# Kernel tuning notes

Measured on AMD Instinct MI355X. Metric: run time of the kernel, lower is better.

The kernel has to match this reference:

```python
import jax, jax.numpy as jnp
import numpy as np

N = 100000      # nodes
E = 1600000     # edges (avg degree 16)
F_IN = 300      # input feature dim
H = 64          # hidden channels
OUT = 20        # output classes
L = 8           # num GCN2Conv layers
ALPHA = 0.1
THETA = 0.5


def setup_inputs() -> dict:
    key = jax.random.key(0)
    ks = jax.random.split(key, 6)
    x = jax.random.normal(ks[0], (N, F_IN), jnp.float32)
    edge_index = jax.random.randint(ks[1], (2, E), 0, N, dtype=jnp.int32)
    edge_weights = jax.random.uniform(ks[2], (E,), jnp.float32)
    W_in = jax.random.normal(ks[3], (F_IN, H), jnp.float32) / np.sqrt(F_IN)
    b_in = jnp.zeros((H,), jnp.float32)
    conv_w = jax.random.normal(ks[4], (L, H, H), jnp.float32) / np.sqrt(H)
    W_out = jax.random.normal(ks[5], (H, OUT), jnp.float32) / np.sqrt(H)
    b_out = jnp.zeros((OUT,), jnp.float32)
    return dict(x=x, edge_index=edge_index, edge_weights=edge_weights,
                W_in=W_in, b_in=b_in, conv_w=conv_w, W_out=W_out, b_out=b_out)


def _gcn_norm(edge_index, edge_weights, n, dtype):
    # add self-loops with weight 1, symmetric normalization (PyG gcn_norm)
    loop = jnp.arange(n, dtype=edge_index.dtype)
    row = jnp.concatenate([edge_index[0], loop])
    col = jnp.concatenate([edge_index[1], loop])
    w = jnp.concatenate([edge_weights, jnp.ones((n,), dtype)])
    deg = jax.ops.segment_sum(w, col, num_segments=n)
    dinv = jnp.where(deg > 0, jax.lax.rsqrt(deg), 0.0).astype(dtype)
    norm = dinv[row] * w * dinv[col]
    return row, col, norm


def reference(x, edge_index, edge_weights, W_in, b_in, conv_w, W_out, b_out):
    n = x.shape[0]
    row, col, norm = _gcn_norm(edge_index, edge_weights, n, x.dtype)
    # eval mode: dropout is identity
    h = jax.nn.relu(x @ W_in + b_in)   # start_with_lin (F_IN != H)
    x0 = h
    num_layers = conv_w.shape[0]
    for l in range(num_layers):
        beta = float(np.log(THETA / (l + 1) + 1.0))
        # A_hat @ h : gather sources, weight by norm, scatter-add to targets
        agg = jax.ops.segment_sum(norm[:, None] * h[row], col, num_segments=n)
        z = (1.0 - ALPHA) * agg + ALPHA * x0  # initial-residual mixing
        h = jax.nn.relu((1.0 - beta) * z + beta * (z @ conv_w[l]))
    return h @ W_out + b_out
```

## Files before the change

### kernel.cpp

```cpp
#include <hip/hip_runtime.h>
#include <hip/hip_fp16.h>
#include <math.h>


#define HID 64
#define FIN 300
#define NOUT 20
#define ALPHA 0.1f
#define DSCALE 262144.0f
#define CNT_SHIFT 25
#define DEG_MASK 0x1FFFFFFu

typedef _Float16 f16;
typedef f16 f16x8 __attribute__((ext_vector_type(8)));
typedef float f32x4 __attribute__((ext_vector_type(4)));

__device__ __forceinline__ float wdec(unsigned v) {
    union { unsigned short u; __half h; } c;
    c.u = (unsigned short)(v >> 17);
    return __half2float(c.h);
}

__device__ __forceinline__ void unpack8(const float4& v, float* f) {
    const __half2* p = reinterpret_cast<const __half2*>(&v);
#pragma unroll
    for (int i = 0; i < 4; ++i) {
        float2 t = __half22float2(p[i]);
        f[2 * i] = t.x;
        f[2 * i + 1] = t.y;
    }
}

__global__ void zero_k(unsigned* __restrict__ p, int nwords) {
    int i = blockIdx.x * blockDim.x + threadIdx.x;
    if (i < nwords) p[i] = 0u;
}

__global__ void accum_k(const int* __restrict__ row, const int* __restrict__ col,
                        const float* __restrict__ w,
                        unsigned* __restrict__ packed8,
                        uint2* __restrict__ rec, int e, int n) {
    int i = blockIdx.x * blockDim.x + threadIdx.x;
    if (i < e) {
        int copy = blockIdx.x & 7;
        int c = col[i], r = row[i];
        float wv = w[i];
        unsigned q = (unsigned)__float2uint_rn(wv * DSCALE);
        unsigned old = atomicAdd(&packed8[(size_t)copy * n + c], (1u << CNT_SHIFT) | q);
        unsigned rank = (old >> CNT_SHIFT) & 0xFFu;
        union { __half h; unsigned short u; } cv;
        cv.h = __float2half(wv);
        rec[i] = make_uint2((unsigned)c | ((unsigned)copy << 17) | (rank << 20),
                            (unsigned)r | ((unsigned)cv.u << 17));
    }
}

__global__ __launch_bounds__(1024) void unpackscan_k(const unsigned* __restrict__ packed8,
                                                     float* __restrict__ dinv,
                                                     unsigned char* __restrict__ off8,
                                                     int* __restrict__ padcnt,
                                                     int* __restrict__ bsum, int n) {
    __shared__ int s[1024];
    int t = threadIdx.x, i = blockIdx.x * 1024 + t;
    int pad = 0;
    if (i < n) {
        unsigned cnt = 0, dsum = 0;
        union { unsigned char b[8]; uint2 u2; } offs;
#pragma unroll
        for (int k = 0; k < 8; ++k) {
            unsigned v = packed8[(size_t)k * n + i];
            offs.b[k] = (unsigned char)cnt;
            cnt += (v >> CNT_SHIFT);
            dsum += (v & DEG_MASK);
        }
        float d = 1.0f + (float)dsum * (1.0f / DSCALE);
        dinv[i] = rsqrtf(d);
        reinterpret_cast<uint2*>(off8)[i] = offs.u2;
        pad = (int)((cnt + 3u) & ~3u);
        padcnt[i] = pad;
    }
    s[t] = pad;
    __syncthreads();
    for (int off = 512; off > 0; off >>= 1) {
        if (t < off) s[t] += s[t + off];
        __syncthreads();
    }
    if (t == 0) bsum[blockIdx.x] = s[0];
}

__global__ void scan2_k(int* __restrict__ bsum, int nb, int* __restrict__ rp, int n) {
    int lane = threadIdx.x;
    int acc = 0;
    for (int base = 0; base < nb; base += 64) {
        int idx = base + lane;
        int orig = (idx < nb) ? bsum[idx] : 0;
        int v = orig;
#pragma unroll
        for (int d = 1; d < 64; d <<= 1) {
            int u = __shfl_up(v, d);
            if (lane >= d) v += u;
        }
        if (idx < nb) bsum[idx] = acc + v - orig;
        acc += __shfl(v, 63);
    }
    if (lane == 0) rp[n] = acc;
}

__global__ __launch_bounds__(1024) void scan3_k(const int* __restrict__ padcnt,
                                                const int* __restrict__ bsum,
                                                int* __restrict__ rp, int n) {
    __shared__ int s[1024];
    int t = threadIdx.x, i = blockIdx.x * 1024 + t;
    int v = (i < n) ? padcnt[i] : 0;
    s[t] = v;
    __syncthreads();
    for (int off = 1; off < 1024; off <<= 1) {
        int u = (t >= off) ? s[t - off] : 0;
        __syncthreads();
        s[t] += u;
        __syncthreads();
    }
    if (i < n) rp[i] = bsum[blockIdx.x] + s[t] - v;
}

__global__ __launch_bounds__(256) void fill_k(const uint2* __restrict__ rec,
                                              const float* __restrict__ dinv,
                                              const int* __restrict__ rp,
                                              const unsigned char* __restrict__ off8,
                                              unsigned* __restrict__ edges,
                                              int e, int n) {
    int xcd = blockIdx.x & 7;
    int lo = (int)(((long long)n * xcd) >> 3);
    int hi = (int)(((long long)n * (xcd + 1)) >> 3);
    int nblk = gridDim.x >> 3;
    int stride = nblk * 256;
    for (int i = (blockIdx.x >> 3) * 256 + threadIdx.x; i < e; i += stride) {
        uint2 rc = rec[i];
        int c = (int)(rc.x & 0x1FFFFu);
        if (c < lo || c >= hi) continue;
        int r = (int)(rc.y & 0x1FFFFu);
        union { unsigned short u; __half h; } ev;
        ev.u = (unsigned short)(rc.y >> 17);
        float nw = (1.0f - ALPHA) * dinv[r] * __half2float(ev.h) * dinv[c];
        union { __half h; unsigned short u; } cv;
        cv.h = __float2half(nw);
        int copy = (int)((rc.x >> 17) & 7u);
        int rank = (int)((rc.x >> 20) & 0xFFu);
        int pos = rp[c] + (int)off8[c * 8 + copy] + rank;
        edges[pos] = ((unsigned)cv.u << 17) | (unsigned)r;
    }
}

__global__ void wt_k(const float* __restrict__ Win, f16* __restrict__ Wt) {
    int i = blockIdx.x * blockDim.x + threadIdx.x;
    if (i < 64 * 320) {
        int c = i / 320, k = i - c * 320;
        Wt[i] = (k < FIN) ? (f16)Win[k * 64 + c] : (f16)0.0f;
    }
}

__global__ __launch_bounds__(256) void gemm_in_k(const float* __restrict__ x,
                                                 const f16* __restrict__ Wt,
                                                 const float* __restrict__ bin,
                                                 __half* __restrict__ x0h, int n) {
    __shared__ f16 As[64 * 72];
    int t = threadIdx.x, lane = t & 63, wv = t >> 6;
    int node0 = blockIdx.x * 64;
    int lr = lane & 15, kg = lane >> 4;
    int fi = t & 15, rowbase = t >> 4;
    f32x4 acc0 = {0, 0, 0, 0}, acc1 = {0, 0, 0, 0}, acc2 = {0, 0, 0, 0}, acc3 = {0, 0, 0, 0};
    float4 xr[4];

    auto loadchunk = [&](int c) {
#pragma unroll
        for (int it = 0; it < 4; ++it) {
            int row = rowbase + it * 16;
            int rr = node0 + row;
            rr = (rr < n) ? rr : (n - 1);
            int kbase = c * 64 + fi * 4;
            xr[it] = make_float4(0.f, 0.f, 0.f, 0.f);
            if (kbase < FIN)
                xr[it] = *reinterpret_cast<const float4*>(x + (size_t)rr * FIN + kbase);
        }
    };
    loadchunk(0);

    for (int c = 0; c < 5; ++c) {
        __syncthreads();
#pragma unroll
        for (int it = 0; it < 4; ++it) {
            int row = rowbase + it * 16;
            union { float2 f2; f16 h[4]; } u;
            u.h[0] = (f16)xr[it].x; u.h[1] = (f16)xr[it].y;
            u.h[2] = (f16)xr[it].z; u.h[3] = (f16)xr[it].w;
            *reinterpret_cast<float2*>(As + row * 72 + fi * 4) = u.f2;
        }
        __syncthreads();
        if (c < 4) loadchunk(c + 1);
#pragma unroll
        for (int ks = 0; ks < 2; ++ks) {
            f16x8 a = *(const f16x8*)(As + (wv * 16 + lr) * 72 + ks * 32 + kg * 8);
            const f16* wb = Wt + c * 64 + ks * 32 + kg * 8;
            f16x8 b0 = *(const f16x8*)(wb + (0 * 16 + lr) * 320);
            f16x8 b1 = *(const f16x8*)(wb + (1 * 16 + lr) * 320);
            f16x8 b2 = *(const f16x8*)(wb + (2 * 16 + lr) * 320);
            f16x8 b3 = *(const f16x8*)(wb + (3 * 16 + lr) * 320);
            acc0 = __builtin_amdgcn_mfma_f32_16x16x32_f16(a, b0, acc0, 0, 0, 0);
            acc1 = __builtin_amdgcn_mfma_f32_16x16x32_f16(a, b1, acc1, 0, 0, 0);
            acc2 = __builtin_amdgcn_mfma_f32_16x16x32_f16(a, b2, acc2, 0, 0, 0);
            acc3 = __builtin_amdgcn_mfma_f32_16x16x32_f16(a, b3, acc3, 0, 0, 0);
        }
    }
    float bi0 = bin[0 * 16 + lr], bi1 = bin[1 * 16 + lr];
    float bi2 = bin[2 * 16 + lr], bi3 = bin[3 * 16 + lr];
    f16 ov[4][4];
#pragma unroll
    for (int r = 0; r < 4; ++r) {
        ov[0][r] = (f16)fmaxf(acc0[r] + bi0, 0.f);
        ov[1][r] = (f16)fmaxf(acc1[r] + bi1, 0.f);
        ov[2][r] = (f16)fmaxf(acc2[r] + bi2, 0.f);
        ov[3][r] = (f16)fmaxf(acc3[r] + bi3, 0.f);
    }
    __syncthreads();
#pragma unroll
    for (int cg = 0; cg < 4; ++cg)
#pragma unroll
        for (int r = 0; r < 4; ++r)
            As[(wv * 16 + kg * 4 + r) * 72 + cg * 16 + lr] = ov[cg][r];
    __syncthreads();
#pragma unroll
    for (int it = 0; it < 2; ++it) {
        int idx = t + it * 256;
        int row = idx >> 3, ch = idx & 7;
        int node = node0 + row;
        if (node < n)
            ((float4*)(x0h + (size_t)node * 64))[ch] =
                *reinterpret_cast<const float4*>(As + row * 72 + ch * 8);
    }
}

__global__ __launch_bounds__(256) void layer_k(const int* __restrict__ rp,
                                               const unsigned* __restrict__ edges,
                                               const float* __restrict__ dinv,
                                               const __half* __restrict__ x0h,
                                               const __half* __restrict__ hin,
                                               __half* __restrict__ hout,
                                               const float* __restrict__ Wl,
                                               float beta, int n,
                                               const float* __restrict__ Wout,
                                               const float* __restrict__ bout,
                                               float* __restrict__ out) {
    __shared__ f16 As[64 * 72];
    __shared__ f16 Bs[64 * 72];
    int t = threadIdx.x, lane = t & 63, wv = t >> 6;
    int node0 = blockIdx.x * 64;
    for (int i = t; i < 4096; i += 256) {
        int k = i >> 6, c = i & 63;
        Bs[c * 72 + k] = (f16)Wl[i];
    }
    int g = lane >> 3, c8 = lane & 7;
#pragma unroll
    for (int pass = 0; pass < 2; ++pass) {
        int row = pass * 32 + wv * 8 + g;
        int node = node0 + row;
        int nd = (node < n) ? node : (n - 1);
        int j = rp[nd], end = (node < n) ? rp[nd + 1] : j;
        float a0[8], a1[8], a2[8], a3[8];
#pragma unroll
        for (int i = 0; i < 8; ++i) { a0[i] = 0.f; a1[i] = 0.f; a2[i] = 0.f; a3[i] = 0.f; }
        while (__any(j < end)) {
            if (j < end) {
                uint4 e4 = *reinterpret_cast<const uint4*>(edges + j);
                float w0 = wdec(e4.x), w1 = wdec(e4.y), w2 = wdec(e4.z), w3 = wdec(e4.w);
                float4 r0 = ((const float4*)(hin + (size_t)(e4.x & 0x1FFFF) * 64))[c8];
                float4 r1 = ((const float4*)(hin + (size_t)(e4.y & 0x1FFFF) * 64))[c8];
                float4 r2 = ((const float4*)(hin + (size_t)(e4.z & 0x1FFFF) * 64))[c8];
                float4 r3 = ((const float4*)(hin + (size_t)(e4.w & 0x1FFFF) * 64))[c8];
                float f0[8], f1[8], f2[8], f3[8];
                unpack8(r0, f0);
                unpack8(r1, f1);
                unpack8(r2, f2);
                unpack8(r3, f3);
#pragma unroll
                for (int i = 0; i < 8; ++i) {
                    a0[i] = fmaf(w0, f0[i], a0[i]);
                    a1[i] = fmaf(w1, f1[i], a1[i]);
                    a2[i] = fmaf(w2, f2[i], a2[i]);
                    a3[i] = fmaf(w3, f3[i], a3[i]);
                }
            }
            j += 4;
        }
        float di = dinv[nd];
        float c1 = (1.0f - ALPHA) * di * di;
        float4 hs4 = ((const float4*)(hin + (size_t)nd * 64))[c8];
        float4 xs4 = ((const float4*)(x0h + (size_t)nd * 64))[c8];
        float hf[8], xf[8];
        unpack8(hs4, hf);
        unpack8(xs4, xf);
        f16x8 zv8;
#pragma unroll
        for (int i = 0; i < 8; ++i)
            zv8[i] = (f16)fmaf(ALPHA, xf[i],
                               fmaf(c1, hf[i], (a0[i] + a1[i]) + (a2[i] + a3[i])));
        *(f16x8*)(As + row * 72 + c8 * 8) = zv8;
    }
    __syncthreads();
    int lr = lane & 15, kg = lane >> 4;
    f32x4 acc0 = {0, 0, 0, 0}, acc1 = {0, 0, 0, 0}, acc2 = {0, 0, 0, 0}, acc3 = {0, 0, 0, 0};
    f16x8 af0 = *(const f16x8*)(As + (wv * 16 + lr) * 72 + kg * 8);
    f16x8 af1 = *(const f16x8*)(As + (wv * 16 + lr) * 72 + 32 + kg * 8);
    {
        f16x8 b0 = *(const f16x8*)(Bs + (0 * 16 + lr) * 72 + kg * 8);
        f16x8 b1 = *(const f16x8*)(Bs + (0 * 16 + lr) * 72 + 32 + kg * 8);
        acc0 = __builtin_amdgcn_mfma_f32_16x16x32_f16(af0, b0, acc0, 0, 0, 0);
        acc0 = __builtin_amdgcn_mfma_f32_16x16x32_f16(af1, b1, acc0, 0, 0, 0);
    }
    {
        f16x8 b0 = *(const f16x8*)(Bs + (1 * 16 + lr) * 72 + kg * 8);
        f16x8 b1 = *(const f16x8*)(Bs + (1 * 16 + lr) * 72 + 32 + kg * 8);
        acc1 = __builtin_amdgcn_mfma_f32_16x16x32_f16(af0, b0, acc1, 0, 0, 0);
        acc1 = __builtin_amdgcn_mfma_f32_16x16x32_f16(af1, b1, acc1, 0, 0, 0);
    }
    {
        f16x8 b0 = *(const f16x8*)(Bs + (2 * 16 + lr) * 72 + kg * 8);
        f16x8 b1 = *(const f16x8*)(Bs + (2 * 16 + lr) * 72 + 32 + kg * 8);
        acc2 = __builtin_amdgcn_mfma_f32_16x16x32_f16(af0, b0, acc2, 0, 0, 0);
        acc2 = __builtin_amdgcn_mfma_f32_16x16x32_f16(af1, b1, acc2, 0, 0, 0);
    }
    {
        f16x8 b0 = *(const f16x8*)(Bs + (3 * 16 + lr) * 72 + kg * 8);
        f16x8 b1 = *(const f16x8*)(Bs + (3 * 16 + lr) * 72 + 32 + kg * 8);
        acc3 = __builtin_amdgcn_mfma_f32_16x16x32_f16(af0, b0, acc3, 0, 0, 0);
        acc3 = __builtin_amdgcn_mfma_f32_16x16x32_f16(af1, b1, acc3, 0, 0, 0);
    }
    float omb = 1.0f - beta;
    f16 ov[4][4];
#pragma unroll
    for (int cg = 0; cg < 4; ++cg) {
        f32x4 acc = (cg == 0) ? acc0 : (cg == 1) ? acc1 : (cg == 2) ? acc2 : acc3;
        int col = cg * 16 + lr;
#pragma unroll
        for (int r = 0; r < 4; ++r) {
            float zv = (float)As[(wv * 16 + kg * 4 + r) * 72 + col];
            ov[cg][r] = (f16)fmaxf(fmaf(beta, acc[r], omb * zv), 0.f);
        }
    }
    __syncthreads();
#pragma unroll
    for (int cg = 0; cg < 4; ++cg)
#pragma unroll
        for (int r = 0; r < 4; ++r)
            As[(wv * 16 + kg * 4 + r) * 72 + cg * 16 + lr] = ov[cg][r];
    __syncthreads();

    if (!Wout) {
#pragma unroll
        for (int it = 0; it < 2; ++it) {
            int idx = t + it * 256;
            int row = idx >> 3, ch = idx & 7;
            int node = node0 + row;
            if (node < n)
                ((float4*)(hout + (size_t)node * 64))[ch] =
                    *reinterpret_cast<const float4*>(As + row * 72 + ch * 8);
        }
    } else {
        for (int i = t; i < 32 * 64; i += 256) {
            int c = i >> 6, k = i & 63;
            Bs[c * 72 + k] = (c < NOUT) ? (f16)Wout[k * NOUT + c] : (f16)0.0f;
        }
        __syncthreads();
        f16x8 ha0 = *(const f16x8*)(As + (wv * 16 + lr) * 72 + kg * 8);
        f16x8 ha1 = *(const f16x8*)(As + (wv * 16 + lr) * 72 + 32 + kg * 8);
#pragma unroll
        for (int ct = 0; ct < 2; ++ct) {
            f32x4 oacc = {0, 0, 0, 0};
            f16x8 b0 = *(const f16x8*)(Bs + (ct * 16 + lr) * 72 + kg * 8);
            f16x8 b1 = *(const f16x8*)(Bs + (ct * 16 + lr) * 72 + 32 + kg * 8);
            oacc = __builtin_amdgcn_mfma_f32_16x16x32_f16(ha0, b0, oacc, 0, 0, 0);
            oacc = __builtin_amdgcn_mfma_f32_16x16x32_f16(ha1, b1, oacc, 0, 0, 0);
            int col = ct * 16 + lr;
            if (col < NOUT) {
                float bo = bout[col];
#pragma unroll
                for (int r = 0; r < 4; ++r) {
                    int node = node0 + wv * 16 + kg * 4 + r;
                    if (node < n) out[(size_t)node * NOUT + col] = oacc[r] + bo;
                }
            }
        }
    }
}

extern "C" void kernel_launch(void* const* d_in, const int* in_sizes, int n_in,
                              void* d_out, int out_size, void* d_ws, size_t ws_size,
                              hipStream_t stream) {
    const float* x    = (const float*)d_in[0];
    const int*   ei   = (const int*)d_in[1];
    const float* ew   = (const float*)d_in[2];
    const float* Win  = (const float*)d_in[3];
    const float* bin  = (const float*)d_in[4];
    const float* cw   = (const float*)d_in[5];
    const float* Wout = (const float*)d_in[6];
    const float* bout = (const float*)d_in[7];

    const int n = in_sizes[0] / FIN;
    const int e = in_sizes[2];
    const int L = in_sizes[5] / (HID * HID);
    const int* row = ei;
    const int* col = ei + e;
    const int epadmax = e + 3 * n + 64;

    size_t off = 0;
    auto alloc = [&](size_t bytes) -> char* {
        char* q = (char*)d_ws + off;
        off = (off + bytes + 255) & ~(size_t)255;
        return q;
    };
    __half* x0h  = (__half*)alloc((size_t)n * HID * 2);
    __half* hA   = (__half*)alloc((size_t)n * HID * 2);
    __half* hB   = (__half*)alloc((size_t)n * HID * 2);
    unsigned* edges = (unsigned*)alloc((size_t)epadmax * 4);
    uint2* rec   = (uint2*)alloc((size_t)e * 8);
    unsigned* packed8 = (unsigned*)alloc((size_t)8 * n * 4);
    unsigned char* off8 = (unsigned char*)alloc((size_t)n * 8);
    float* dinv  = (float*)alloc((size_t)n * 4);
    int*   padcnt= (int*)alloc((size_t)n * 4);
    int*   rp    = (int*)alloc((size_t)(n + 1) * 4);
    int*   bsum  = (int*)alloc(1024 * 4);
    f16*   Wt    = (f16*)alloc((size_t)64 * 320 * 2);

    const int nb = (n + 1023) / 1024;
    const int ntile = (n + 63) / 64;

    zero_k<<<(8 * n + 255) / 256, 256, 0, stream>>>(packed8, 8 * n);
    zero_k<<<(epadmax + 255) / 256, 256, 0, stream>>>(edges, epadmax);
    accum_k<<<(e + 255) / 256, 256, 0, stream>>>(row, col, ew, packed8, rec, e, n);
    unpackscan_k<<<nb, 1024, 0, stream>>>(packed8, dinv, off8, padcnt, bsum, n);
    scan2_k<<<1, 64, 0, stream>>>(bsum, nb, rp, n);
    scan3_k<<<nb, 1024, 0, stream>>>(padcnt, bsum, rp, n);
    fill_k<<<1024, 256, 0, stream>>>(rec, dinv, rp, off8, edges, e, n);

    wt_k<<<(64 * 320 + 255) / 256, 256, 0, stream>>>(Win, Wt);
    gemm_in_k<<<ntile, 256, 0, stream>>>(x, Wt, bin, x0h, n);

    const __half* hin = x0h;
    __half* hout = hA;
    for (int l = 0; l < L; ++l) {
        float beta = (float)log(0.5 / (double)(l + 1) + 1.0);
        bool last = (l == L - 1);
        layer_k<<<ntile, 256, 0, stream>>>(rp, edges, dinv, x0h, hin, hout,
                                           cw + (size_t)l * HID * HID, beta, n,
                                           last ? Wout : nullptr,
                                           last ? bout : nullptr,
                                           last ? (float*)d_out : nullptr);
        hin = hout;
        hout = (hout == hA) ? hB : hA;
    }
}
```

Baseline: 492.0 us.

## Store features in quarter-split layout, single degree counter, warp-shuffle scans

Node features move from a row-major [n][64] layout to four column slabs of 16 halves each. The layer kernel now runs four passes, one per slab, with 4 lanes per node and 16 nodes per wave, so each gather touches a smaller working set. The eight-copy atomic degree/count array and its offset table are replaced by one packed counter per node, with the rank field cut to 7 bits. The block scans now use wave shuffles, and the zero kernels become hipMemsetAsync calls. The trade-off is that the edge list is walked four times per layer, and a node whose in-degree exceeds 127 would have its rank overflow into other bits.

```diff
diff --git a/kernel.cpp b/kernel.cpp
--- a/kernel.cpp
+++ b/kernel.cpp
@@ -12,6 +12,7 @@
 #define DEG_MASK 0x1FFFFFFu
 
 typedef _Float16 f16;
+typedef f16 f16x4 __attribute__((ext_vector_type(4)));
 typedef f16 f16x8 __attribute__((ext_vector_type(8)));
 typedef float f32x4 __attribute__((ext_vector_type(4)));
 
@@ -21,71 +22,50 @@
     return __half2float(c.h);
 }
 
-__device__ __forceinline__ void unpack8(const float4& v, float* f) {
-    const __half2* p = reinterpret_cast<const __half2*>(&v);
-#pragma unroll
-    for (int i = 0; i < 4; ++i) {
-        float2 t = __half22float2(p[i]);
-        f[2 * i] = t.x;
-        f[2 * i + 1] = t.y;
-    }
-}
-
-__global__ void zero_k(unsigned* __restrict__ p, int nwords) {
-    int i = blockIdx.x * blockDim.x + threadIdx.x;
-    if (i < nwords) p[i] = 0u;
-}
-
 __global__ void accum_k(const int* __restrict__ row, const int* __restrict__ col,
-                        const float* __restrict__ w,
-                        unsigned* __restrict__ packed8,
-                        uint2* __restrict__ rec, int e, int n) {
+                        const float* __restrict__ ew,
+                        unsigned* __restrict__ packed,
+                        uint2* __restrict__ rec, int e) {
     int i = blockIdx.x * blockDim.x + threadIdx.x;
     if (i < e) {
-        int copy = blockIdx.x & 7;
         int c = col[i], r = row[i];
-        float wv = w[i];
+        float wv = ew[i];
         unsigned q = (unsigned)__float2uint_rn(wv * DSCALE);
-        unsigned old = atomicAdd(&packed8[(size_t)copy * n + c], (1u << CNT_SHIFT) | q);
-        unsigned rank = (old >> CNT_SHIFT) & 0xFFu;
+        unsigned old = atomicAdd(&packed[c], (1u << CNT_SHIFT) | q);
+        unsigned rank = (old >> CNT_SHIFT) & 0x7Fu;
         union { __half h; unsigned short u; } cv;
         cv.h = __float2half(wv);
-        rec[i] = make_uint2((unsigned)c | ((unsigned)copy << 17) | (rank << 20),
+        rec[i] = make_uint2((unsigned)c | (rank << 17),
                             (unsigned)r | ((unsigned)cv.u << 17));
     }
 }
 
-__global__ __launch_bounds__(1024) void unpackscan_k(const unsigned* __restrict__ packed8,
+__global__ __launch_bounds__(1024) void unpackscan_k(const unsigned* __restrict__ packed,
                                                      float* __restrict__ dinv,
-                                                     unsigned char* __restrict__ off8,
                                                      int* __restrict__ padcnt,
                                                      int* __restrict__ bsum, int n) {
-    __shared__ int s[1024];
+    __shared__ int ws[16];
     int t = threadIdx.x, i = blockIdx.x * 1024 + t;
     int pad = 0;
     if (i < n) {
-        unsigned cnt = 0, dsum = 0;
-        union { unsigned char b[8]; uint2 u2; } offs;
-#pragma unroll
-        for (int k = 0; k < 8; ++k) {
-            unsigned v = packed8[(size_t)k * n + i];
-            offs.b[k] = (unsigned char)cnt;
-            cnt += (v >> CNT_SHIFT);
-            dsum += (v & DEG_MASK);
-        }
-        float d = 1.0f + (float)dsum * (1.0f / DSCALE);
+        unsigned v = packed[i];
+        int cnt = (int)(v >> CNT_SHIFT);
+        float d = 1.0f + (float)(v & DEG_MASK) * (1.0f / DSCALE);
         dinv[i] = rsqrtf(d);
-        reinterpret_cast<uint2*>(off8)[i] = offs.u2;
-        pad = (int)((cnt + 3u) & ~3u);
+        pad = (cnt + 3) & ~3;
         padcnt[i] = pad;
     }
-    s[t] = pad;
-    __syncthreads();
-    for (int off = 512; off > 0; off >>= 1) {
-        if (t < off) s[t] += s[t + off];
-        __syncthreads();
-    }
-    if (t == 0) bsum[blockIdx.x] = s[0];
+    int s = pad;
+#pragma unroll
+    for (int d = 1; d < 64; d <<= 1) s += __shfl_xor(s, d);
+    if ((t & 63) == 0) ws[t >> 6] = s;
+    __syncthreads();
+    if (t == 0) {
+        int tot = 0;
+#pragma unroll
+        for (int k = 0; k < 16; ++k) tot += ws[k];
+        bsum[blockIdx.x] = tot;
+    }
 }
 
 __global__ void scan2_k(int* __restrict__ bsum, int nb, int* __restrict__ rp, int n) {
@@ -109,24 +89,35 @@
 __global__ __launch_bounds__(1024) void scan3_k(const int* __restrict__ padcnt,
                                                 const int* __restrict__ bsum,
                                                 int* __restrict__ rp, int n) {
-    __shared__ int s[1024];
+    __shared__ int ws[16];
     int t = threadIdx.x, i = blockIdx.x * 1024 + t;
+    int lane = t & 63, w = t >> 6;
     int v = (i < n) ? padcnt[i] : 0;
-    s[t] = v;
-    __syncthreads();
-    for (int off = 1; off < 1024; off <<= 1) {
-        int u = (t >= off) ? s[t - off] : 0;
-        __syncthreads();
-        s[t] += u;
-        __syncthreads();
-    }
-    if (i < n) rp[i] = bsum[blockIdx.x] + s[t] - v;
+    int sv = v;
+#pragma unroll
+    for (int d = 1; d < 64; d <<= 1) {
+        int u = __shfl_up(sv, d);
+        if (lane >= d) sv += u;
+    }
+    if (lane == 63) ws[w] = sv;
+    __syncthreads();
+    if (w == 0) {
+        int x = (lane < 16) ? ws[lane] : 0;
+#pragma unroll
+        for (int d = 1; d < 16; d <<= 1) {
+            int u = __shfl_up(x, d);
+            if (lane >= d) x += u;
+        }
+        if (lane < 16) ws[lane] = x;
+    }
+    __syncthreads();
+    int woff = (w > 0) ? ws[w - 1] : 0;
+    if (i < n) rp[i] = bsum[blockIdx.x] + woff + sv - v;
 }
 
 __global__ __launch_bounds__(256) void fill_k(const uint2* __restrict__ rec,
                                               const float* __restrict__ dinv,
                                               const int* __restrict__ rp,
-                                              const unsigned char* __restrict__ off8,
                                               unsigned* __restrict__ edges,
                                               int e, int n) {
     int xcd = blockIdx.x & 7;
@@ -144,9 +135,8 @@
         float nw = (1.0f - ALPHA) * dinv[r] * __half2float(ev.h) * dinv[c];
         union { __half h; unsigned short u; } cv;
         cv.h = __float2half(nw);
-        int copy = (int)((rc.x >> 17) & 7u);
-        int rank = (int)((rc.x >> 20) & 0xFFu);
-        int pos = rp[c] + (int)off8[c * 8 + copy] + rank;
+        int rank = (int)((rc.x >> 17) & 0x7Fu);
+        int pos = rp[c] + rank;
         edges[pos] = ((unsigned)cv.u << 17) | (unsigned)r;
     }
 }
@@ -231,11 +221,11 @@
 #pragma unroll
     for (int it = 0; it < 2; ++it) {
         int idx = t + it * 256;
-        int row = idx >> 3, ch = idx & 7;
-        int node = node0 + row;
+        int sub = idx & 1, nodel = (idx >> 1) & 63, q = idx >> 7;
+        int node = node0 + nodel;
         if (node < n)
-            ((float4*)(x0h + (size_t)node * 64))[ch] =
-                *reinterpret_cast<const float4*>(As + row * 72 + ch * 8);
+            *(float4*)((f16*)x0h + ((size_t)q * n + node) * 16 + sub * 8) =
+                *reinterpret_cast<const float4*>(As + nodel * 72 + q * 16 + sub * 8);
     }
 }
 
@@ -258,52 +248,47 @@
         int k = i >> 6, c = i & 63;
         Bs[c * 72 + k] = (f16)Wl[i];
     }
-    int g = lane >> 3, c8 = lane & 7;
-#pragma unroll
-    for (int pass = 0; pass < 2; ++pass) {
-        int row = pass * 32 + wv * 8 + g;
-        int node = node0 + row;
-        int nd = (node < n) ? node : (n - 1);
-        int j = rp[nd], end = (node < n) ? rp[nd + 1] : j;
-        float a0[8], a1[8], a2[8], a3[8];
-#pragma unroll
-        for (int i = 0; i < 8; ++i) { a0[i] = 0.f; a1[i] = 0.f; a2[i] = 0.f; a3[i] = 0.f; }
+    int g = lane >> 2, s = lane & 3;
+    int row = wv * 16 + g;
+    int node = node0 + row;
+    int nd = (node < n) ? node : (n - 1);
+    int jbeg = rp[nd], end = (node < n) ? rp[nd + 1] : jbeg;
+    float di = dinv[nd];
+    float c1 = (1.0f - ALPHA) * di * di;
+#pragma unroll
+    for (int q = 0; q < 4; ++q) {
+        const f16* hp = (const f16*)hin + (size_t)q * n * 16;
+        const f16* xp = (const f16*)x0h + (size_t)q * n * 16;
+        float a0[4], a1[4], a2[4], a3[4];
+#pragma unroll
+        for (int i = 0; i < 4; ++i) { a0[i] = 0.f; a1[i] = 0.f; a2[i] = 0.f; a3[i] = 0.f; }
+        int j = jbeg;
         while (__any(j < end)) {
             if (j < end) {
                 uint4 e4 = *reinterpret_cast<const uint4*>(edges + j);
                 float w0 = wdec(e4.x), w1 = wdec(e4.y), w2 = wdec(e4.z), w3 = wdec(e4.w);
-                float4 r0 = ((const float4*)(hin + (size_t)(e4.x & 0x1FFFF) * 64))[c8];
-                float4 r1 = ((const float4*)(hin + (size_t)(e4.y & 0x1FFFF) * 64))[c8];
-                float4 r2 = ((const float4*)(hin + (size_t)(e4.z & 0x1FFFF) * 64))[c8];
-                float4 r3 = ((const float4*)(hin + (size_t)(e4.w & 0x1FFFF) * 64))[c8];
-                float f0[8], f1[8], f2[8], f3[8];
-                unpack8(r0, f0);
-                unpack8(r1, f1);
-                unpack8(r2, f2);
-                unpack8(r3, f3);
-#pragma unroll
-                for (int i = 0; i < 8; ++i) {
-                    a0[i] = fmaf(w0, f0[i], a0[i]);
-                    a1[i] = fmaf(w1, f1[i], a1[i]);
-                    a2[i] = fmaf(w2, f2[i], a2[i]);
-                    a3[i] = fmaf(w3, f3[i], a3[i]);
+                f16x4 r0 = *(const f16x4*)(hp + (size_t)(e4.x & 0x1FFFF) * 16 + s * 4);
+                f16x4 r1 = *(const f16x4*)(hp + (size_t)(e4.y & 0x1FFFF) * 16 + s * 4);
+                f16x4 r2 = *(const f16x4*)(hp + (size_t)(e4.z & 0x1FFFF) * 16 + s * 4);
+                f16x4 r3 = *(const f16x4*)(hp + (size_t)(e4.w & 0x1FFFF) * 16 + s * 4);
+#pragma unroll
+                for (int i = 0; i < 4; ++i) {
+                    a0[i] = fmaf(w0, (float)r0[i], a0[i]);
+                    a1[i] = fmaf(w1, (float)r1[i], a1[i]);
+                    a2[i] = fmaf(w2, (float)r2[i], a2[i]);
+                    a3[i] = fmaf(w3, (float)r3[i], a3[i]);
                 }
             }
             j += 4;
         }
-        float di = dinv[nd];
-        float c1 = (1.0f - ALPHA) * di * di;
-        float4 hs4 = ((const float4*)(hin + (size_t)nd * 64))[c8];
-        float4 xs4 = ((const float4*)(x0h + (size_t)nd * 64))[c8];
-        float hf[8], xf[8];
-        unpack8(hs4, hf);
-        unpack8(xs4, xf);
-        f16x8 zv8;
-#pragma unroll
-        for (int i = 0; i < 8; ++i)
-            zv8[i] = (f16)fmaf(ALPHA, xf[i],
-                               fmaf(c1, hf[i], (a0[i] + a1[i]) + (a2[i] + a3[i])));
-        *(f16x8*)(As + row * 72 + c8 * 8) = zv8;
+        f16x4 h4 = *(const f16x4*)(hp + (size_t)nd * 16 + s * 4);
+        f16x4 x4 = *(const f16x4*)(xp + (size_t)nd * 16 + s * 4);
+        f16x4 z4;
+#pragma unroll
+        for (int i = 0; i < 4; ++i)
+            z4[i] = (f16)fmaf(ALPHA, (float)x4[i],
+                              fmaf(c1, (float)h4[i], (a0[i] + a1[i]) + (a2[i] + a3[i])));
+        *(f16x4*)(As + row * 72 + q * 16 + s * 4) = z4;
     }
     __syncthreads();
     int lr = lane & 15, kg = lane >> 4;
@@ -358,11 +343,11 @@
 #pragma unroll
         for (int it = 0; it < 2; ++it) {
             int idx = t + it * 256;
-            int row = idx >> 3, ch = idx & 7;
-            int node = node0 + row;
-            if (node < n)
-                ((float4*)(hout + (size_t)node * 64))[ch] =
-                    *reinterpret_cast<const float4*>(As + row * 72 + ch * 8);
+            int sub = idx & 1, nodel = (idx >> 1) & 63, q = idx >> 7;
+            int nd2 = node0 + nodel;
+            if (nd2 < n)
+                *(float4*)((f16*)hout + ((size_t)q * n + nd2) * 16 + sub * 8) =
+                    *reinterpret_cast<const float4*>(As + nodel * 72 + q * 16 + sub * 8);
         }
     } else {
         for (int i = t; i < 32 * 64; i += 256) {
@@ -384,8 +369,8 @@
                 float bo = bout[col];
 #pragma unroll
                 for (int r = 0; r < 4; ++r) {
-                    int node = node0 + wv * 16 + kg * 4 + r;
-                    if (node < n) out[(size_t)node * NOUT + col] = oacc[r] + bo;
+                    int nd2 = node0 + wv * 16 + kg * 4 + r;
+                    if (nd2 < n) out[(size_t)nd2 * NOUT + col] = oacc[r] + bo;
                 }
             }
         }
@@ -422,8 +407,7 @@
     __half* hB   = (__half*)alloc((size_t)n * HID * 2);
     unsigned* edges = (unsigned*)alloc((size_t)epadmax * 4);
     uint2* rec   = (uint2*)alloc((size_t)e * 8);
-    unsigned* packed8 = (unsigned*)alloc((size_t)8 * n * 4);
-    unsigned char* off8 = (unsigned char*)alloc((size_t)n * 8);
+    unsigned* packed = (unsigned*)alloc((size_t)n * 4);
     float* dinv  = (float*)alloc((size_t)n * 4);
     int*   padcnt= (int*)alloc((size_t)n * 4);
     int*   rp    = (int*)alloc((size_t)(n + 1) * 4);
@@ -433,13 +417,13 @@
     const int nb = (n + 1023) / 1024;
     const int ntile = (n + 63) / 64;
 
-    zero_k<<<(8 * n + 255) / 256, 256, 0, stream>>>(packed8, 8 * n);
-    zero_k<<<(epadmax + 255) / 256, 256, 0, stream>>>(edges, epadmax);
-    accum_k<<<(e + 255) / 256, 256, 0, stream>>>(row, col, ew, packed8, rec, e, n);
-    unpackscan_k<<<nb, 1024, 0, stream>>>(packed8, dinv, off8, padcnt, bsum, n);
+    hipMemsetAsync(packed, 0, (size_t)n * 4, stream);
+    hipMemsetAsync(edges, 0, (size_t)epadmax * 4, stream);
+    accum_k<<<(e + 255) / 256, 256, 0, stream>>>(row, col, ew, packed, rec, e);
+    unpackscan_k<<<nb, 1024, 0, stream>>>(packed, dinv, padcnt, bsum, n);
     scan2_k<<<1, 64, 0, stream>>>(bsum, nb, rp, n);
     scan3_k<<<nb, 1024, 0, stream>>>(padcnt, bsum, rp, n);
-    fill_k<<<1024, 256, 0, stream>>>(rec, dinv, rp, off8, edges, e, n);
+    fill_k<<<1024, 256, 0, stream>>>(rec, dinv, rp, edges, e, n);
 
     wt_k<<<(64 * 320 + 255) / 256, 256, 0, stream>>>(Win, Wt);
     gemm_in_k<<<ntile, 256, 0, stream>>>(x, Wt, bin, x0h, n);
```

Measured after the change: 780.8 us. 58.7% more time.
